# Kernel tuning notes

Hardware: AMD Instinct MI355X
Metric: run time of the kernel (lower is better)

The kernel has to match this reference:

```python
import jax, jax.numpy as jnp
import numpy as np

B, L, D, V = 4096, 200, 64, 100000
ATTR_LEN = (2, 6, 10)  # label_size = 18
NEG = -1e9


def setup_inputs() -> dict:
    key = jax.random.key(0)
    ks = jax.random.split(key, 12)
    x = jax.random.randint(ks[0], (B, L), 0, V)
    lengths = jax.random.randint(ks[1], (B,), 1, L + 1)  # ragged valid lengths >= 1
    x_mask = jnp.arange(L)[None, :] < lengths[:, None]   # prefix-valid bool mask [B,L]
    y = (jax.random.uniform(ks[2], (B, sum(ATTR_LEN))) < 0.5).astype(jnp.float32)
    ob = (jax.random.uniform(ks[3], (B, sum(ATTR_LEN))) < 0.8).astype(jnp.float32)
    emb_table = (jax.random.normal(ks[4], (V, D)) * 0.02).at[0].set(0.0)  # padding_idx=0
    tran_W = jax.random.normal(ks[5], (3, D, D)) * 0.05   # emb_tran Linear weights (per attr)
    tran_b = jnp.zeros((3, D))
    att_W = jax.random.normal(ks[6], (3, D)) * 0.05       # item_att_W: Linear(D,1) per attr
    att_b = jnp.zeros((3,))
    W0 = jax.random.normal(ks[7], (D, ATTR_LEN[0])) * 0.05  # W_all (no bias)
    W1 = jax.random.normal(ks[8], (D, ATTR_LEN[1])) * 0.05
    W2 = jax.random.normal(ks[9], (D, ATTR_LEN[2])) * 0.05
    return {"x": x, "x_mask": x_mask, "y": y, "ob": ob, "emb_table": emb_table,
            "tran_W": tran_W, "tran_b": tran_b, "att_W": att_W, "att_b": att_b,
            "W0": W0, "W1": W1, "W2": W2}


def reference(x, x_mask, y, ob, emb_table, tran_W, tran_b, att_W, att_b, W0, W1, W2):
    # embed: [B,L,D]
    embed = emb_table[x]
    # per-attribute transformed embeddings: [3,B,L,D]
    e = jax.nn.relu(jnp.einsum('bld,ade->able', embed, tran_W) + tran_b[:, None, None, :])
    # attention logits per attribute: [3,B,L]
    att_u = jax.nn.relu(jnp.einsum('able,ae->abl', e, att_W) + att_b[:, None, None])
    # masked softmax over valid prefix (equivalent to the per-sample length loop)
    m = x_mask.astype(e.dtype)
    scores = jnp.where(x_mask[None, :, :], att_u, NEG)
    att = jax.nn.softmax(scores, axis=-1) * m[None, :, :]
    # attention-pooled user representation per attribute: [3,B,D]
    rep = jnp.tanh(jnp.einsum('abl,able->abe', att, e))
    # torch: cat([rep_a.unsqueeze(2)],2).view(B,-1) -> interleaved (d-major, attr-minor) layout
    user_flat = jnp.transpose(rep, (1, 2, 0)).reshape(rep.shape[1], -1)  # [B, 3*D]
    Ddim = emb_table.shape[1]
    W_user = jnp.concatenate([user_flat[:, 0 * Ddim:1 * Ddim] @ W0,
                              user_flat[:, 1 * Ddim:2 * Ddim] @ W1,
                              user_flat[:, 2 * Ddim:3 * Ddim] @ W2], axis=1)
    # W_compact = W_user * ob  (observed-label mask)
    return W_user * ob
```

## Files before the change

### kernel.cpp

```cpp
#include <hip/hip_runtime.h>

typedef unsigned int u32;
typedef unsigned short u16;
typedef unsigned char u8;
typedef unsigned long long u64;

typedef __attribute__((ext_vector_type(8))) short bf16x8;
typedef __attribute__((ext_vector_type(4))) float f32x4;
typedef __attribute__((ext_vector_type(4))) u32 u32x4;

#define L_SEQ 200
#define ST_ROWS 208
#define RND_MAX 9

__device__ __forceinline__ u16 f2bf(float f) {
    u32 u = __float_as_uint(f);
    return (u16)((u + 0x7FFFu + ((u >> 16) & 1u)) >> 16);
}
__device__ __forceinline__ u32 pk2bf(float fx, float fy) {
    u32 xb = __float_as_uint(fx) + 0x8000u;
    u32 yb = __float_as_uint(fy) + 0x8000u;
    return __byte_perm(xb, yb, 0x7632);
}

__device__ __forceinline__ void gld_lds16(const void* g, void* l) {
    __builtin_amdgcn_global_load_lds(
        (const __attribute__((address_space(1))) u32*)g,
        (__attribute__((address_space(3))) u32*)l, 16, 0, 0);
}

__device__ __forceinline__ float row16_sum(float v) {
    int x;
    x = __builtin_amdgcn_update_dpp(0, __float_as_int(v), 0x128, 0xF, 0xF, true);
    v += __int_as_float(x);
    x = __builtin_amdgcn_update_dpp(0, __float_as_int(v), 0x124, 0xF, 0xF, true);
    v += __int_as_float(x);
    x = __builtin_amdgcn_update_dpp(0, __float_as_int(v), 0x122, 0xF, 0xF, true);
    v += __int_as_float(x);
    x = __builtin_amdgcn_update_dpp(0, __float_as_int(v), 0x121, 0xF, 0xF, true);
    v += __int_as_float(x);
    return v;
}
__device__ __forceinline__ float wave_sumf(float v) {
    v = row16_sum(v);
    v += __shfl_xor(v, 16, 64);
    v += __shfl_xor(v, 32, 64);
    return v;
}

__global__ __launch_bounds__(256) void etna_prep(const void* __restrict__ xmask,
                                                 const float* __restrict__ tranW,
                                                 const float* __restrict__ emb,
                                                 void* __restrict__ ws, int Bn, int Vn,
                                                 int doConv) {
    const int tid = threadIdx.x;
    const int bid = blockIdx.x;

    if (doConv) {
        u64* dst = (u64*)((char*)ws + 40960);
        const float4* src = (const float4*)emb;
        int ng = Vn * 16;
        for (int i = bid * 256 + tid; i < ng; i += gridDim.x * 256) {
            float4 v = src[i];
            u64 lo = pk2bf(v.x, v.y);
            u64 hi = pk2bf(v.z, v.w);
            dst[i] = lo | (hi << 32);
        }
    }

    if (bid < 48) {
        int it = bid * 256 + tid;
        int jj = it & 7;
        int ln = (it >> 3) & 63;
        int kh = (it >> 9) & 1;
        int c = (it >> 10) & 3;
        int a = it >> 12;
        int k = kh * 32 + (ln >> 4) * 8 + jj;
        int n = c * 16 + (ln & 15);
        ((u16*)ws)[it] = f2bf(tranW[a * 4096 + k * 64 + n]);
        return;
    }

    const int wv = tid >> 6;
    const int lane = tid & 63;
    int esz;
    {
        u32 accF = 0, acc0 = 0, accO = 0;
#pragma unroll
        for (int k = 0; k < 4; ++k) {
            int i = lane + 64 * k;
            u32 w = (i < 200) ? ((const u32*)xmask)[i] : 0u;
            accF |= (w & 0xFEFEFEFEu);
            acc0 |= (w & 0x000000FFu);
            accO |= (w & 0xFFFFFF00u);
        }
        bool isFloat = __ballot(accF != 0) != 0;
        bool hasB0   = __ballot(acc0 != 0) != 0;
        bool hasOdd  = __ballot(accO != 0) != 0;
        esz = isFloat ? (hasB0 ? 2 : 4) : (hasOdd ? 1 : 4);
    }
    int s = (bid - 48) * 4 + wv;
    if (s < Bn) {
        int len = 0;
        int mbase = s * L_SEQ;
#pragma unroll
        for (int c4 = 0; c4 < 4; ++c4) {
            int l = c4 * 64 + lane;
            bool v = false;
            if (l < L_SEQ) {
                int off = mbase + l;
                if (esz == 1)      v = ((const u8*)xmask)[off] != 0;
                else if (esz == 2) v = ((const u16*)xmask)[off] != 0;
                else               v = ((const u32*)xmask)[off] != 0;
            }
            len += (int)__popcll(__ballot(v));
        }
        if (lane == 0) ((int*)((char*)ws + 24576))[s] = len;
    }
}

template <bool TAB>
__global__ __launch_bounds__(192, 4) void etna_mfma(
    const int* __restrict__ x, const float* __restrict__ ob,
    const float* __restrict__ emb, const float* __restrict__ tranb,
    const float* __restrict__ attW, const float* __restrict__ attb,
    const float* __restrict__ W0, const float* __restrict__ W1,
    const float* __restrict__ W2, float* __restrict__ out,
    const void* __restrict__ ws, int Vn) {
    __shared__ __align__(16) float ldsf[ST_ROWS * 32];
    __shared__ float rep[3][64];
    char* ldsb = (char*)ldsf;

    const int tid = threadIdx.x;
    const int a = tid >> 6;
    const int lane = tid & 63;
    const int col = lane & 15;
    const int g = lane >> 4;
    const int b = blockIdx.x;

    const u16* wsBf = (const u16*)ws;
    bf16x8 Bf[4][2];
#pragma unroll
    for (int c = 0; c < 4; ++c)
#pragma unroll
        for (int kh = 0; kh < 2; ++kh)
            Bf[c][kh] = *(const bf16x8*)&wsBf[(((a * 4 + c) * 2 + kh) * 64 + lane) * 8];

    const int len = ((const int*)((const char*)ws + 24576))[b];
    const u16* wsEmb = (const u16*)((const char*)ws + 40960);

    const float LOG2E = 1.44269504088896f;
    float TB[4], AW[4];
#pragma unroll
    for (int c = 0; c < 4; ++c) {
        TB[c] = tranb[a * 64 + c * 16 + col];
        AW[c] = attW[a * 64 + c * 16 + col] * LOG2E;
    }
    const float AB = attb[a] * LOG2E;

    const int* xrow = x + b * L_SEQ;
    const int nt = (len + 15) >> 4;
    const int stRows = nt << 4;
    const int rounds = (stRows + 23) / 24;

    const int sp = a * 8 + (lane >> 3);
    const int ch = lane & 7;
    const u32 srcChunkOff = (u32)((ch ^ (lane >> 3)) << 4);

    int ids[RND_MAX];
#pragma unroll
    for (int j = 0; j < RND_MAX; ++j) {
        ids[j] = 0;
        if (j < rounds) {
            int p = j * 24 + sp;
            int q = (p < L_SEQ) ? p : (L_SEQ - 1);
            int idv = xrow[q];
            idv = max(0, min(idv, Vn - 1));
            ids[j] = (p < len) ? idv : 0;
        }
    }

    if (TAB) {
#pragma unroll
        for (int j = 0; j < RND_MAX; ++j) {
            if (j < rounds) {
                int p = j * 24 + sp;
                const char* gsrc =
                    (const char*)wsEmb + (size_t)ids[j] * 128 + srcChunkOff;
                char* ldst = ldsb + (u32)(j * 24 + a * 8) * 128;
                if (p < stRows)
                    gld_lds16(gsrc, ldst);
            }
        }
    } else {
        for (int j = 0; j < rounds; ++j) {
            int p = j * 24 + sp;
            if (p < stRows) {
                const float4* ep4 = (const float4*)(emb + (size_t)ids[j] * 64);
                float4 q0 = ep4[2 * ch], q1 = ep4[2 * ch + 1];
                u32x4 wv_;
                wv_.x = pk2bf(q0.x, q0.y);
                wv_.y = pk2bf(q0.z, q0.w);
                wv_.z = pk2bf(q1.x, q1.y);
                wv_.w = pk2bf(q1.z, q1.w);
                u32 off = (u32)p * 128 + (u32)((ch * 16) ^ ((p & 7) << 4));
                *(bf16x8*)(ldsb + off) = __builtin_bit_cast(bf16x8, wv_);
            }
        }
    }
    __syncthreads();

    const u32 c0 = (u32)((g * 16) ^ ((col & 7) << 4));
    u32 ra = (u32)col * 128 + c0;

    float NUM[4] = {0.f, 0.f, 0.f, 0.f};
    float DEN = 0.f;

    bf16x8 a0 = *(const bf16x8*)(ldsb + ra);
    bf16x8 a1 = *(const bf16x8*)(ldsb + (ra ^ 64u));

    for (int t = 0; t < nt; ++t) {
        bf16x8 n0 = a0, n1 = a1;
        if (t + 1 < nt) {
            u32 rn = ra + 2048u;
            n0 = *(const bf16x8*)(ldsb + rn);
            n1 = *(const bf16x8*)(ldsb + (rn ^ 64u));
        }
        ra += 2048u;

        f32x4 E[4];
#pragma unroll
        for (int c = 0; c < 4; ++c) {
            f32x4 cc = {TB[c], TB[c], TB[c], TB[c]};
            cc = __builtin_amdgcn_mfma_f32_16x16x32_bf16(a0, Bf[c][0], cc, 0, 0, 0);
            cc = __builtin_amdgcn_mfma_f32_16x16x32_bf16(a1, Bf[c][1], cc, 0, 0, 0);
            E[c].x = fmaxf(cc.x, 0.f);
            E[c].y = fmaxf(cc.y, 0.f);
            E[c].z = fmaxf(cc.z, 0.f);
            E[c].w = fmaxf(cc.w, 0.f);
        }
        float p0 = E[0].x * AW[0] + E[1].x * AW[1] + E[2].x * AW[2] + E[3].x * AW[3];
        float p1 = E[0].y * AW[0] + E[1].y * AW[1] + E[2].y * AW[2] + E[3].y * AW[3];
        float p2 = E[0].z * AW[0] + E[1].z * AW[1] + E[2].z * AW[2] + E[3].z * AW[3];
        float p3 = E[0].w * AW[0] + E[1].w * AW[1] + E[2].w * AW[2] + E[3].w * AW[3];
        p0 = row16_sum(p0);
        p1 = row16_sum(p1);
        p2 = row16_sum(p2);
        p3 = row16_sum(p3);

        float s0 = exp2f(fmaxf(p0 + AB, 0.f));
        float s1 = exp2f(fmaxf(p1 + AB, 0.f));
        float s2 = exp2f(fmaxf(p2 + AB, 0.f));
        float s3 = exp2f(fmaxf(p3 + AB, 0.f));
        if (t == nt - 1) {
            int lrow = (t << 4) + 4 * g;
            s0 = (lrow + 0 < len) ? s0 : 0.f;
            s1 = (lrow + 1 < len) ? s1 : 0.f;
            s2 = (lrow + 2 < len) ? s2 : 0.f;
            s3 = (lrow + 3 < len) ? s3 : 0.f;
        }
        DEN += s0 + s1 + s2 + s3;
#pragma unroll
        for (int c = 0; c < 4; ++c)
            NUM[c] += s0 * E[c].x + s1 * E[c].y + s2 * E[c].z + s3 * E[c].w;

        a0 = n0;
        a1 = n1;
    }

    {
        float d = DEN;
        d += __shfl_xor(d, 16, 64);
        d += __shfl_xor(d, 32, 64);
        float rden = 1.0f / fmaxf(d, 1e-20f);
#pragma unroll
        for (int c = 0; c < 4; ++c) {
            float v = NUM[c];
            v += __shfl_xor(v, 16, 64);
            v += __shfl_xor(v, 32, 64);
            if (g == 0) rep[a][c * 16 + col] = tanhf(v * rden);
        }
    }
    __syncthreads();

#pragma unroll
    for (int r = 0; r < 6; ++r) {
        int o = a + 3 * r;
        int seg = (o < 2) ? 0 : ((o < 8) ? 1 : 2);
        int k = o - ((seg == 0) ? 0 : ((seg == 1) ? 2 : 8));
        int AL = (seg == 0) ? 2 : ((seg == 1) ? 6 : 10);
        const float* Wp = (seg == 0) ? W0 : ((seg == 1) ? W1 : W2);
        int gg = seg * 64 + lane;
        float v = rep[gg % 3][gg / 3];
        float pz = wave_sumf(v * Wp[lane * AL + k]);
        if (lane == 0) out[b * 18 + o] = pz * ob[b * 18 + o];
    }
}

extern "C" void kernel_launch(void* const* d_in, const int* in_sizes, int n_in,
                              void* d_out, int out_size, void* d_ws, size_t ws_size,
                              hipStream_t stream) {
    const int* x = (const int*)d_in[0];
    const void* xmask = d_in[1];
    const float* ob = (const float*)d_in[3];
    const float* emb = (const float*)d_in[4];
    const float* tranW = (const float*)d_in[5];
    const float* tranb = (const float*)d_in[6];
    const float* attW = (const float*)d_in[7];
    const float* attb = (const float*)d_in[8];
    const float* W0 = (const float*)d_in[9];
    const float* W1 = (const float*)d_in[10];
    const float* W2 = (const float*)d_in[11];

    const int Bn = in_sizes[0] / L_SEQ;
    const int Vn = in_sizes[4] / 64;

    const size_t need = 40960 + (size_t)Vn * 128;
    const int useTab = (ws_size >= need) ? 1 : 0;

    etna_prep<<<48 + (Bn + 3) / 4, 256, 0, stream>>>(xmask, tranW, emb, d_ws, Bn, Vn, useTab);
    if (useTab)
        etna_mfma<true><<<Bn, 192, 0, stream>>>(x, ob, emb, tranb, attW, attb,
                                                W0, W1, W2, (float*)d_out, d_ws, Vn);
    else
        etna_mfma<false><<<Bn, 192, 0, stream>>>(x, ob, emb, tranb, attW, attb,
                                                 W0, W1, W2, (float*)d_out, d_ws, Vn);
}
```

Baseline: 144.1 us.

## Fuse prep into main kernel and gather fp32 embeddings directly with software pipelining

Removes the separate prep kernel. That kernel converted the whole 100k-row embedding table to bf16 in workspace, repacked tranW, and computed per-sample lengths. Now each block computes its own length from the mask, builds the bf16 B fragments from fp32 tranW directly, and gathers only the needed fp32 embedding rows, converting them in registers. The gather uses a 3-deep register pipeline before the swizzled LDS stores. This drops a full-table conversion pass and a kernel launch, at the cost of redundant per-block tranW loads and twice the gather bytes per row.

```diff
diff --git a/kernel.cpp b/kernel.cpp
--- a/kernel.cpp
+++ b/kernel.cpp
@@ -11,7 +11,7 @@
 
 #define L_SEQ 200
 #define ST_ROWS 208
-#define RND_MAX 9
+#define RND9 9
 
 __device__ __forceinline__ u16 f2bf(float f) {
     u32 u = __float_as_uint(f);
@@ -21,12 +21,6 @@
     u32 xb = __float_as_uint(fx) + 0x8000u;
     u32 yb = __float_as_uint(fy) + 0x8000u;
     return __byte_perm(xb, yb, 0x7632);
-}
-
-__device__ __forceinline__ void gld_lds16(const void* g, void* l) {
-    __builtin_amdgcn_global_load_lds(
-        (const __attribute__((address_space(1))) u32*)g,
-        (__attribute__((address_space(3))) u32*)l, 16, 0, 0);
 }
 
 __device__ __forceinline__ float row16_sum(float v) {
@@ -48,41 +42,24 @@
     return v;
 }
 
-__global__ __launch_bounds__(256) void etna_prep(const void* __restrict__ xmask,
-                                                 const float* __restrict__ tranW,
-                                                 const float* __restrict__ emb,
-                                                 void* __restrict__ ws, int Bn, int Vn,
-                                                 int doConv) {
+__global__ __launch_bounds__(192, 4) void etna_fused(
+    const int* __restrict__ x, const void* __restrict__ xmask,
+    const float* __restrict__ ob, const float* __restrict__ emb,
+    const float* __restrict__ tranW, const float* __restrict__ tranb,
+    const float* __restrict__ attW, const float* __restrict__ attb,
+    const float* __restrict__ W0, const float* __restrict__ W1,
+    const float* __restrict__ W2, float* __restrict__ out, int Vn) {
+    __shared__ __align__(16) float ldsf[ST_ROWS * 32];
+    __shared__ float rep[3][64];
+    char* ldsb = (char*)ldsf;
+
     const int tid = threadIdx.x;
-    const int bid = blockIdx.x;
-
-    if (doConv) {
-        u64* dst = (u64*)((char*)ws + 40960);
-        const float4* src = (const float4*)emb;
-        int ng = Vn * 16;
-        for (int i = bid * 256 + tid; i < ng; i += gridDim.x * 256) {
-            float4 v = src[i];
-            u64 lo = pk2bf(v.x, v.y);
-            u64 hi = pk2bf(v.z, v.w);
-            dst[i] = lo | (hi << 32);
-        }
-    }
-
-    if (bid < 48) {
-        int it = bid * 256 + tid;
-        int jj = it & 7;
-        int ln = (it >> 3) & 63;
-        int kh = (it >> 9) & 1;
-        int c = (it >> 10) & 3;
-        int a = it >> 12;
-        int k = kh * 32 + (ln >> 4) * 8 + jj;
-        int n = c * 16 + (ln & 15);
-        ((u16*)ws)[it] = f2bf(tranW[a * 4096 + k * 64 + n]);
-        return;
-    }
-
-    const int wv = tid >> 6;
+    const int a = tid >> 6;
     const int lane = tid & 63;
+    const int col = lane & 15;
+    const int g = lane >> 4;
+    const int b = blockIdx.x;
+
     int esz;
     {
         u32 accF = 0, acc0 = 0, accO = 0;
@@ -99,10 +76,10 @@
         bool hasOdd  = __ballot(accO != 0) != 0;
         esz = isFloat ? (hasB0 ? 2 : 4) : (hasOdd ? 1 : 4);
     }
-    int s = (bid - 48) * 4 + wv;
-    if (s < Bn) {
-        int len = 0;
-        int mbase = s * L_SEQ;
+
+    int len = 0;
+    {
+        int mbase = b * L_SEQ;
 #pragma unroll
         for (int c4 = 0; c4 < 4; ++c4) {
             int l = c4 * 64 + lane;
@@ -115,39 +92,23 @@
             }
             len += (int)__popcll(__ballot(v));
         }
-        if (lane == 0) ((int*)((char*)ws + 24576))[s] = len;
-    }
-}
-
-template <bool TAB>
-__global__ __launch_bounds__(192, 4) void etna_mfma(
-    const int* __restrict__ x, const float* __restrict__ ob,
-    const float* __restrict__ emb, const float* __restrict__ tranb,
-    const float* __restrict__ attW, const float* __restrict__ attb,
-    const float* __restrict__ W0, const float* __restrict__ W1,
-    const float* __restrict__ W2, float* __restrict__ out,
-    const void* __restrict__ ws, int Vn) {
-    __shared__ __align__(16) float ldsf[ST_ROWS * 32];
-    __shared__ float rep[3][64];
-    char* ldsb = (char*)ldsf;
-
-    const int tid = threadIdx.x;
-    const int a = tid >> 6;
-    const int lane = tid & 63;
-    const int col = lane & 15;
-    const int g = lane >> 4;
-    const int b = blockIdx.x;
-
-    const u16* wsBf = (const u16*)ws;
+    }
+
     bf16x8 Bf[4][2];
 #pragma unroll
     for (int c = 0; c < 4; ++c)
 #pragma unroll
-        for (int kh = 0; kh < 2; ++kh)
-            Bf[c][kh] = *(const bf16x8*)&wsBf[(((a * 4 + c) * 2 + kh) * 64 + lane) * 8];
-
-    const int len = ((const int*)((const char*)ws + 24576))[b];
-    const u16* wsEmb = (const u16*)((const char*)ws + 40960);
+        for (int kh = 0; kh < 2; ++kh) {
+            const float* tp = tranW + a * 4096 + (kh * 32 + g * 8) * 64 + c * 16 + col;
+            u32x4 wv_;
+#pragma unroll
+            for (int m = 0; m < 4; ++m) {
+                float f0 = tp[(2 * m) * 64];
+                float f1 = tp[(2 * m + 1) * 64];
+                wv_[m] = (u32)f2bf(f0) | ((u32)f2bf(f1) << 16);
+            }
+            Bf[c][kh] = __builtin_bit_cast(bf16x8, wv_);
+        }
 
     const float LOG2E = 1.44269504088896f;
     float TB[4], AW[4];
@@ -163,16 +124,16 @@
     const int stRows = nt << 4;
     const int rounds = (stRows + 23) / 24;
 
-    const int sp = a * 8 + (lane >> 3);
-    const int ch = lane & 7;
-    const u32 srcChunkOff = (u32)((ch ^ (lane >> 3)) << 4);
-
-    int ids[RND_MAX];
-#pragma unroll
-    for (int j = 0; j < RND_MAX; ++j) {
+    const int rs = tid >> 3;
+    const int ch8 = tid & 7;
+    const u32 swz = (u32)((ch8 ^ (rs & 7)) << 4);
+
+    int ids[RND9];
+#pragma unroll
+    for (int j = 0; j < RND9; ++j) {
         ids[j] = 0;
         if (j < rounds) {
-            int p = j * 24 + sp;
+            int p = j * 24 + rs;
             int q = (p < L_SEQ) ? p : (L_SEQ - 1);
             int idv = xrow[q];
             idv = max(0, min(idv, Vn - 1));
@@ -180,31 +141,27 @@
         }
     }
 
-    if (TAB) {
-#pragma unroll
-        for (int j = 0; j < RND_MAX; ++j) {
-            if (j < rounds) {
-                int p = j * 24 + sp;
-                const char* gsrc =
-                    (const char*)wsEmb + (size_t)ids[j] * 128 + srcChunkOff;
-                char* ldst = ldsb + (u32)(j * 24 + a * 8) * 128;
-                if (p < stRows)
-                    gld_lds16(gsrc, ldst);
-            }
-        }
-    } else {
-        for (int j = 0; j < rounds; ++j) {
-            int p = j * 24 + sp;
-            if (p < stRows) {
-                const float4* ep4 = (const float4*)(emb + (size_t)ids[j] * 64);
-                float4 q0 = ep4[2 * ch], q1 = ep4[2 * ch + 1];
-                u32x4 wv_;
-                wv_.x = pk2bf(q0.x, q0.y);
-                wv_.y = pk2bf(q0.z, q0.w);
-                wv_.z = pk2bf(q1.x, q1.y);
-                wv_.w = pk2bf(q1.z, q1.w);
-                u32 off = (u32)p * 128 + (u32)((ch * 16) ^ ((p & 7) << 4));
-                *(bf16x8*)(ldsb + off) = __builtin_bit_cast(bf16x8, wv_);
+    {
+        float4 fq[3][2];
+#pragma unroll
+        for (int j = 0; j < RND9 + 2; ++j) {
+            if (j < RND9 && j < rounds) {
+                const float* rp = emb + (size_t)ids[j] * 64 + ch8 * 8;
+                fq[j % 3][0] = *(const float4*)(rp);
+                fq[j % 3][1] = *(const float4*)(rp + 4);
+            }
+            int k = j - 2;
+            if (k >= 0 && k < rounds) {
+                int p = k * 24 + rs;
+                if (p < stRows) {
+                    u32x4 wv_;
+                    wv_.x = pk2bf(fq[k % 3][0].x, fq[k % 3][0].y);
+                    wv_.y = pk2bf(fq[k % 3][0].z, fq[k % 3][0].w);
+                    wv_.z = pk2bf(fq[k % 3][1].x, fq[k % 3][1].y);
+                    wv_.w = pk2bf(fq[k % 3][1].z, fq[k % 3][1].w);
+                    u32 off = (u32)p * 128 + swz;
+                    *(bf16x8*)(ldsb + off) = __builtin_bit_cast(bf16x8, wv_);
+                }
             }
         }
     }
@@ -315,14 +272,6 @@
     const int Bn = in_sizes[0] / L_SEQ;
     const int Vn = in_sizes[4] / 64;
 
-    const size_t need = 40960 + (size_t)Vn * 128;
-    const int useTab = (ws_size >= need) ? 1 : 0;
-
-    etna_prep<<<48 + (Bn + 3) / 4, 256, 0, stream>>>(xmask, tranW, emb, d_ws, Bn, Vn, useTab);
-    if (useTab)
-        etna_mfma<true><<<Bn, 192, 0, stream>>>(x, ob, emb, tranb, attW, attb,
-                                                W0, W1, W2, (float*)d_out, d_ws, Vn);
-    else
-        etna_mfma<false><<<Bn, 192, 0, stream>>>(x, ob, emb, tranb, attW, attb,
-                                                 W0, W1, W2, (float*)d_out, d_ws, Vn);
-}
+    etna_fused<<<Bn, 192, 0, stream>>>(x, xmask, ob, emb, tranW, tranb, attW,
+                                       attb, W0, W1, W2, (float*)d_out, Vn);
+}
```

New measurement: 162.7 us. 12.9% more time.

## Stage embeddings in two smaller LDS passes to double occupancy

Applied to the files above, without the earlier changes.

The LDS staging buffer shrinks from 208 rows to 112 rows (7 tiles), and the sequence is processed in passes of at most 7 tiles, each gathering its embeddings, syncing, and running the MFMA/softmax accumulation. Launch bounds rise from 4 to 8 waves-groups per SIMD so more blocks fit per CU and latency hiding improves. In exchange, long sequences need two gather/compute phases with an extra barrier, so the second gather is not overlapped within the block, and register pressure is capped more tightly.

```diff
diff --git a/kernel.cpp b/kernel.cpp
--- a/kernel.cpp
+++ b/kernel.cpp
@@ -10,8 +10,9 @@
 typedef __attribute__((ext_vector_type(4))) u32 u32x4;
 
 #define L_SEQ 200
-#define ST_ROWS 208
-#define RND_MAX 9
+#define PASS_TILES 7
+#define PASS_ROWS 112
+#define RND5 5
 
 __device__ __forceinline__ u16 f2bf(float f) {
     u32 u = __float_as_uint(f);
@@ -120,14 +121,14 @@
 }
 
 template <bool TAB>
-__global__ __launch_bounds__(192, 4) void etna_mfma(
+__global__ __launch_bounds__(192, 8) void etna_mfma(
     const int* __restrict__ x, const float* __restrict__ ob,
     const float* __restrict__ emb, const float* __restrict__ tranb,
     const float* __restrict__ attW, const float* __restrict__ attb,
     const float* __restrict__ W0, const float* __restrict__ W1,
     const float* __restrict__ W2, float* __restrict__ out,
     const void* __restrict__ ws, int Vn) {
-    __shared__ __align__(16) float ldsf[ST_ROWS * 32];
+    __shared__ __align__(16) float ldsf[PASS_ROWS * 32];
     __shared__ float rep[3][64];
     char* ldsb = (char*)ldsf;
 
@@ -160,112 +161,119 @@
 
     const int* xrow = x + b * L_SEQ;
     const int nt = (len + 15) >> 4;
-    const int stRows = nt << 4;
-    const int rounds = (stRows + 23) / 24;
 
     const int sp = a * 8 + (lane >> 3);
     const int ch = lane & 7;
     const u32 srcChunkOff = (u32)((ch ^ (lane >> 3)) << 4);
 
-    int ids[RND_MAX];
-#pragma unroll
-    for (int j = 0; j < RND_MAX; ++j) {
-        ids[j] = 0;
-        if (j < rounds) {
-            int p = j * 24 + sp;
-            int q = (p < L_SEQ) ? p : (L_SEQ - 1);
-            int idv = xrow[q];
-            idv = max(0, min(idv, Vn - 1));
-            ids[j] = (p < len) ? idv : 0;
-        }
-    }
-
-    if (TAB) {
-#pragma unroll
-        for (int j = 0; j < RND_MAX; ++j) {
-            if (j < rounds) {
-                int p = j * 24 + sp;
-                const char* gsrc =
-                    (const char*)wsEmb + (size_t)ids[j] * 128 + srcChunkOff;
-                char* ldst = ldsb + (u32)(j * 24 + a * 8) * 128;
-                if (p < stRows)
-                    gld_lds16(gsrc, ldst);
-            }
-        }
-    } else {
-        for (int j = 0; j < rounds; ++j) {
-            int p = j * 24 + sp;
-            if (p < stRows) {
-                const float4* ep4 = (const float4*)(emb + (size_t)ids[j] * 64);
-                float4 q0 = ep4[2 * ch], q1 = ep4[2 * ch + 1];
-                u32x4 wv_;
-                wv_.x = pk2bf(q0.x, q0.y);
-                wv_.y = pk2bf(q0.z, q0.w);
-                wv_.z = pk2bf(q1.x, q1.y);
-                wv_.w = pk2bf(q1.z, q1.w);
-                u32 off = (u32)p * 128 + (u32)((ch * 16) ^ ((p & 7) << 4));
-                *(bf16x8*)(ldsb + off) = __builtin_bit_cast(bf16x8, wv_);
-            }
-        }
-    }
-    __syncthreads();
-
     const u32 c0 = (u32)((g * 16) ^ ((col & 7) << 4));
-    u32 ra = (u32)col * 128 + c0;
 
     float NUM[4] = {0.f, 0.f, 0.f, 0.f};
     float DEN = 0.f;
 
-    bf16x8 a0 = *(const bf16x8*)(ldsb + ra);
-    bf16x8 a1 = *(const bf16x8*)(ldsb + (ra ^ 64u));
-
-    for (int t = 0; t < nt; ++t) {
-        bf16x8 n0 = a0, n1 = a1;
-        if (t + 1 < nt) {
-            u32 rn = ra + 2048u;
-            n0 = *(const bf16x8*)(ldsb + rn);
-            n1 = *(const bf16x8*)(ldsb + (rn ^ 64u));
-        }
-        ra += 2048u;
-
-        f32x4 E[4];
-#pragma unroll
-        for (int c = 0; c < 4; ++c) {
-            f32x4 cc = {TB[c], TB[c], TB[c], TB[c]};
-            cc = __builtin_amdgcn_mfma_f32_16x16x32_bf16(a0, Bf[c][0], cc, 0, 0, 0);
-            cc = __builtin_amdgcn_mfma_f32_16x16x32_bf16(a1, Bf[c][1], cc, 0, 0, 0);
-            E[c].x = fmaxf(cc.x, 0.f);
-            E[c].y = fmaxf(cc.y, 0.f);
-            E[c].z = fmaxf(cc.z, 0.f);
-            E[c].w = fmaxf(cc.w, 0.f);
-        }
-        float p0 = E[0].x * AW[0] + E[1].x * AW[1] + E[2].x * AW[2] + E[3].x * AW[3];
-        float p1 = E[0].y * AW[0] + E[1].y * AW[1] + E[2].y * AW[2] + E[3].y * AW[3];
-        float p2 = E[0].z * AW[0] + E[1].z * AW[1] + E[2].z * AW[2] + E[3].z * AW[3];
-        float p3 = E[0].w * AW[0] + E[1].w * AW[1] + E[2].w * AW[2] + E[3].w * AW[3];
-        p0 = row16_sum(p0);
-        p1 = row16_sum(p1);
-        p2 = row16_sum(p2);
-        p3 = row16_sum(p3);
-
-        float s0 = exp2f(fmaxf(p0 + AB, 0.f));
-        float s1 = exp2f(fmaxf(p1 + AB, 0.f));
-        float s2 = exp2f(fmaxf(p2 + AB, 0.f));
-        float s3 = exp2f(fmaxf(p3 + AB, 0.f));
-        if (t == nt - 1) {
-            int lrow = (t << 4) + 4 * g;
-            s0 = (lrow + 0 < len) ? s0 : 0.f;
-            s1 = (lrow + 1 < len) ? s1 : 0.f;
-            s2 = (lrow + 2 < len) ? s2 : 0.f;
-            s3 = (lrow + 3 < len) ? s3 : 0.f;
-        }
-        DEN += s0 + s1 + s2 + s3;
-#pragma unroll
-        for (int c = 0; c < 4; ++c)
-            NUM[c] += s0 * E[c].x + s1 * E[c].y + s2 * E[c].z + s3 * E[c].w;
-
-        a0 = n0;
-        a1 = n1;
+    for (int base = 0; base < nt; base += PASS_TILES) {
+        const int tEnd = min(nt, base + PASS_TILES);
+        const int rowsPass = (tEnd - base) << 4;
+        const int rp = (rowsPass + 23) / 24;
+        const int row0 = base << 4;
+
+        int ids[RND5];
+#pragma unroll
+        for (int j = 0; j < RND5; ++j) {
+            ids[j] = 0;
+            if (j < rp) {
+                int p = row0 + j * 24 + sp;
+                int q = (p < L_SEQ) ? p : (L_SEQ - 1);
+                int idv = xrow[q];
+                idv = max(0, min(idv, Vn - 1));
+                ids[j] = (p < len) ? idv : 0;
+            }
+        }
+
+        if (TAB) {
+#pragma unroll
+            for (int j = 0; j < RND5; ++j) {
+                if (j < rp) {
+                    int lp = j * 24 + sp;
+                    const char* gsrc =
+                        (const char*)wsEmb + (size_t)ids[j] * 128 + srcChunkOff;
+                    char* ldst = ldsb + (u32)(j * 24 + a * 8) * 128;
+                    if (lp < rowsPass)
+                        gld_lds16(gsrc, ldst);
+                }
+            }
+        } else {
+            for (int j = 0; j < rp; ++j) {
+                int lp = j * 24 + sp;
+                if (lp < rowsPass) {
+                    const float4* ep4 = (const float4*)(emb + (size_t)ids[j] * 64);
+                    float4 q0 = ep4[2 * ch], q1 = ep4[2 * ch + 1];
+                    u32x4 wv_;
+                    wv_.x = pk2bf(q0.x, q0.y);
+                    wv_.y = pk2bf(q0.z, q0.w);
+                    wv_.z = pk2bf(q1.x, q1.y);
+                    wv_.w = pk2bf(q1.z, q1.w);
+                    u32 off = (u32)lp * 128 + (u32)((ch * 16) ^ ((lp & 7) << 4));
+                    *(bf16x8*)(ldsb + off) = __builtin_bit_cast(bf16x8, wv_);
+                }
+            }
+        }
+        __syncthreads();
+
+        u32 ra = (u32)col * 128 + c0;
+        bf16x8 a0 = *(const bf16x8*)(ldsb + ra);
+        bf16x8 a1 = *(const bf16x8*)(ldsb + (ra ^ 64u));
+
+        for (int t = base; t < tEnd; ++t) {
+            bf16x8 n0 = a0, n1 = a1;
+            if (t + 1 < tEnd) {
+                u32 rn = ra + 2048u;
+                n0 = *(const bf16x8*)(ldsb + rn);
+                n1 = *(const bf16x8*)(ldsb + (rn ^ 64u));
+            }
+            ra += 2048u;
+
+            f32x4 E[4];
+#pragma unroll
+            for (int c = 0; c < 4; ++c) {
+                f32x4 cc = {TB[c], TB[c], TB[c], TB[c]};
+                cc = __builtin_amdgcn_mfma_f32_16x16x32_bf16(a0, Bf[c][0], cc, 0, 0, 0);
+                cc = __builtin_amdgcn_mfma_f32_16x16x32_bf16(a1, Bf[c][1], cc, 0, 0, 0);
+                E[c].x = fmaxf(cc.x, 0.f);
+                E[c].y = fmaxf(cc.y, 0.f);
+                E[c].z = fmaxf(cc.z, 0.f);
+                E[c].w = fmaxf(cc.w, 0.f);
+            }
+            float p0 = E[0].x * AW[0] + E[1].x * AW[1] + E[2].x * AW[2] + E[3].x * AW[3];
+            float p1 = E[0].y * AW[0] + E[1].y * AW[1] + E[2].y * AW[2] + E[3].y * AW[3];
+            float p2 = E[0].z * AW[0] + E[1].z * AW[1] + E[2].z * AW[2] + E[3].z * AW[3];
+            float p3 = E[0].w * AW[0] + E[1].w * AW[1] + E[2].w * AW[2] + E[3].w * AW[3];
+            p0 = row16_sum(p0);
+            p1 = row16_sum(p1);
+            p2 = row16_sum(p2);
+            p3 = row16_sum(p3);
+
+            float s0 = exp2f(fmaxf(p0 + AB, 0.f));
+            float s1 = exp2f(fmaxf(p1 + AB, 0.f));
+            float s2 = exp2f(fmaxf(p2 + AB, 0.f));
+            float s3 = exp2f(fmaxf(p3 + AB, 0.f));
+            if (t == nt - 1) {
+                int lrow = (t << 4) + 4 * g;
+                s0 = (lrow + 0 < len) ? s0 : 0.f;
+                s1 = (lrow + 1 < len) ? s1 : 0.f;
+                s2 = (lrow + 2 < len) ? s2 : 0.f;
+                s3 = (lrow + 3 < len) ? s3 : 0.f;
+            }
+            DEN += s0 + s1 + s2 + s3;
+#pragma unroll
+            for (int c = 0; c < 4; ++c)
+                NUM[c] += s0 * E[c].x + s1 * E[c].y + s2 * E[c].z + s3 * E[c].w;
+
+            a0 = n0;
+            a1 = n1;
+        }
+
+        if (tEnd < nt) __syncthreads();
     }
 
     {
```

After: 236.2 us. 63.9% more time.
